# Optimization experiments

Measured on AMD Instinct MI355X. Metric: run time of the kernel, lower is better.

Reference implementation:

```python
import jax, jax.numpy as jnp
import numpy as np
from jax import lax

BS, NT, CH, K = 8, 128, 1024, 4
H = 512  # num_output_chanls // 2 per direction (bidirectional)
G = 4 * H  # gate dim, PyTorch order i,f,g,o


def setup_inputs() -> dict:
    key = jax.random.key(0)
    ks = jax.random.split(key, 9)
    s = 1.0 / np.sqrt(H)
    u = lambda k_, shape: jax.random.uniform(k_, shape, jnp.float32, -s, s)
    return {
        "inputs": jax.random.normal(ks[0], (BS, NT, CH, K), jnp.float32),
        "Wih_f": u(ks[1], (K, G, CH)),
        "Whh_f": u(ks[2], (K, G, H)),
        "bih_f": u(ks[3], (K, G)),
        "bhh_f": u(ks[4], (K, G)),
        "Wih_b": u(ks[5], (K, G, CH)),
        "Whh_b": u(ks[6], (K, G, H)),
        "bih_b": u(ks[7], (K, G)),
        "bhh_b": u(ks[8], (K, G)),
    }


def _lstm_dir(x_tbck, Wih, Whh, bih, bhh, reverse):
    # x_tbck: [nt, bs, ch, k]; weights batched over k heads.
    bs = x_tbck.shape[1]
    k, _, h = Whh.shape
    bias = bih + bhh  # [k, 4h]

    def step(carry, x_t):
        h_prev, c_prev = carry
        # detach_hidden_state=True: hidden state detached each step
        h_prev = lax.stop_gradient(h_prev)
        c_prev = lax.stop_gradient(c_prev)
        gates = (jnp.einsum('bck,kgc->bkg', x_t, Wih)
                 + jnp.einsum('bkh,kgh->bkg', h_prev, Whh)
                 + bias)  # [bs, k, 4h]
        i, f, g, o = jnp.split(gates, 4, axis=-1)
        c_new = jax.nn.sigmoid(f) * c_prev + jax.nn.sigmoid(i) * jnp.tanh(g)
        h_new = jax.nn.sigmoid(o) * jnp.tanh(c_new)
        return (h_new, c_new), h_new

    init = (jnp.zeros((bs, k, h), x_tbck.dtype), jnp.zeros((bs, k, h), x_tbck.dtype))
    _, hs = lax.scan(step, init, x_tbck, reverse=reverse)  # [nt, bs, k, h]
    return hs


def reference(inputs, Wih_f, Whh_f, bih_f, bhh_f, Wih_b, Whh_b, bih_b, bhh_b):
    # inputs: [bs, nt, ch, k] -> scan over time
    x = jnp.transpose(inputs, (1, 0, 2, 3))  # [nt, bs, ch, k]
    hs_f = _lstm_dir(x, Wih_f, Whh_f, bih_f, bhh_f, reverse=False)
    hs_b = _lstm_dir(x, Wih_b, Whh_b, bih_b, bhh_b, reverse=True)
    # [nt, bs, k, h] -> [bs, nt, h, k]; concat forward/backward on hidden dim
    hs_f = jnp.transpose(hs_f, (1, 0, 3, 2))
    hs_b = jnp.transpose(hs_b, (1, 0, 3, 2))
    return jnp.concatenate([hs_f, hs_b], axis=2)  # [bs, nt, 2h, k]
```

## Files before the change

### kernel.cpp

```cpp
#include <hip/hip_runtime.h>
#include <stdint.h>


typedef __attribute__((ext_vector_type(8))) short short8;
typedef __attribute__((ext_vector_type(4))) float floatx4;
typedef unsigned long long ull;

#define POISON 0x7FC07FC07FC07FC0ull

#define GLOAD_LDS16(g, l)                                        \
  __builtin_amdgcn_global_load_lds(                              \
      (const __attribute__((address_space(1))) void*)(g),        \
      (__attribute__((address_space(3))) void*)(l), 16, 0, 0)

__device__ __forceinline__ unsigned short f2bf(float f) {
  unsigned u = __float_as_uint(f);
  u = (u + 0x7fffu + ((u >> 16) & 1u)) >> 16;
  return (unsigned short)u;
}
__device__ __forceinline__ float sigm(float x) { return 1.0f / (1.0f + __expf(-x)); }
__device__ __forceinline__ float tanh_f(float x) {
  float ax = fabsf(x);
  float e = __expf(-2.0f * ax);
  float t = (1.0f - e) / (1.0f + e);
  return x < 0.0f ? -t : t;
}

__global__ void pack_x_k(const float* __restrict__ x, unsigned short* __restrict__ Xp) {
  int g = blockIdx.x * 256 + threadIdx.x;
  int m = g >> 10, c = g & 1023;
  int t = m >> 3, b = m & 7;
  float4 v = *(const float4*)(x + ((size_t)((b * 128 + t) * 1024 + c)) * 4);
  Xp[g]           = f2bf(v.x);
  Xp[1048576 + g] = f2bf(v.y);
  Xp[2097152 + g] = f2bf(v.z);
  Xp[3145728 + g] = f2bf(v.w);
}

__global__ void cast_bf_k(const float* __restrict__ src, unsigned short* __restrict__ dst, int n4) {
  int i = blockIdx.x * 256 + threadIdx.x;
  if (i >= n4) return;
  float4 v = ((const float4*)src)[i];
  ushort4 o;
  o.x = f2bf(v.x); o.y = f2bf(v.y); o.z = f2bf(v.z); o.w = f2bf(v.w);
  ((ushort4*)dst)[i] = o;
}

__global__ void bias_k(const float* __restrict__ bihf, const float* __restrict__ bhhf,
                       const float* __restrict__ bihb, const float* __restrict__ bhhb,
                       float* __restrict__ bias) {
  int i = blockIdx.x * 256 + threadIdx.x;
  int dk = i >> 11, g = i & 2047, kk = dk & 3;
  const float* a = (dk < 4) ? bihf : bihb;
  const float* b = (dk < 4) ? bhhf : bhhb;
  bias[i] = a[kk * 2048 + g] + b[kk * 2048 + g];
}

__global__ void fill_poison_k(ull* __restrict__ p) {
  p[(size_t)blockIdx.x * 256 + threadIdx.x] = POISON;
}

__global__ __launch_bounds__(256) void gemm_ih_k(
    const unsigned short* __restrict__ Xp, const unsigned short* __restrict__ Wb,
    const float* __restrict__ bias, float* __restrict__ ih) {
  const int mt = blockIdx.x, ntl = blockIdx.y, dk = blockIdx.z;
  const int kh = dk & 3;
  const int tid = threadIdx.x;
  const int L = tid & 63, w = tid >> 6;
  const int wm = w & 1, wn = w >> 1;
  const int quad = L >> 4, lo = L & 15;

  __shared__ unsigned short As[128 * 32];
  __shared__ unsigned short Bs[128 * 32];

  const unsigned short* Ab = Xp + (size_t)kh * 1048576 + (size_t)mt * 128 * 1024;
  const unsigned short* Bb = Wb + (size_t)dk * 2097152 + (size_t)ntl * 128 * 1024;

  floatx4 acc[4][4] = {};

  for (int kc = 0; kc < 32; ++kc) {
#pragma unroll
    for (int q = 0; q < 2; ++q) {
      int c = q * 256 + w * 64 + L;
      int ldsb = (q * 256 + w * 64) * 8;
      GLOAD_LDS16(Ab + (size_t)(c >> 2) * 1024 + kc * 32 + (c & 3) * 8, As + ldsb);
      GLOAD_LDS16(Bb + (size_t)(c >> 2) * 1024 + kc * 32 + (c & 3) * 8, Bs + ldsb);
    }
    __syncthreads();
    short8 af[4], bf[4];
#pragma unroll
    for (int mi = 0; mi < 4; ++mi)
      af[mi] = *(const short8*)(As + (wm * 64 + mi * 16 + lo) * 32 + quad * 8);
#pragma unroll
    for (int ni = 0; ni < 4; ++ni)
      bf[ni] = *(const short8*)(Bs + (wn * 64 + ni * 16 + lo) * 32 + quad * 8);
#pragma unroll
    for (int mi = 0; mi < 4; ++mi)
#pragma unroll
      for (int ni = 0; ni < 4; ++ni)
        acc[mi][ni] = __builtin_amdgcn_mfma_f32_16x16x32_bf16(af[mi], bf[ni], acc[mi][ni], 0, 0, 0);
    __syncthreads();
  }

#pragma unroll
  for (int mi = 0; mi < 4; ++mi)
#pragma unroll
    for (int ni = 0; ni < 4; ++ni) {
      int g = ntl * 128 + wn * 64 + ni * 16 + lo;
      float bv = bias[dk * 2048 + g];
#pragma unroll
      for (int r = 0; r < 4; ++r) {
        int m = mt * 128 + wm * 64 + mi * 16 + quad * 4 + r;
        ih[((size_t)dk * 1024 + m) * 2048 + g] = acc[mi][ni][r] + bv;
      }
    }
}

__global__ __launch_bounds__(256) void lstm_rec_k(
    const float* __restrict__ ih, const unsigned short* __restrict__ whh,
    float* __restrict__ out, ull* __restrict__ stateS) {
  const int tid = threadIdx.x;
  const int L = tid & 63;
  const int w = tid >> 6;
  const int grp = blockIdx.x & 7;
  const int d = grp >> 2, kh = grp & 3;
  const int wg = blockIdx.x >> 3;
  const int j0 = wg * 32;
  const int quad = L >> 4, lo = L & 15;

  __shared__ unsigned short h_lds[16 * 520];
  __shared__ float gbuf[4][8][32];

  for (int i = tid; i < 16 * 520; i += 256) h_lds[i] = 0;

  short8 bfrag[2][16];
#pragma unroll
  for (int ni = 0; ni < 2; ++ni) {
    const unsigned short* wb =
        whh + ((size_t)grp * 2048 + (size_t)(w * 512 + j0 + ni * 16 + lo)) * 512 + quad * 8;
#pragma unroll
    for (int kk = 0; kk < 16; ++kk) bfrag[ni][kk] = *(const short8*)(wb + kk * 32);
  }

  const int pb = tid >> 5, pjj = tid & 31;
  float creg = 0.0f;

  float ihv[2][4];
  {
    int t0 = d ? 127 : 0;
#pragma unroll
    for (int ni = 0; ni < 2; ++ni) {
      const float* ihp =
          ih + ((size_t)grp * 1024 + (size_t)t0 * 8) * 2048 + (w * 512 + j0 + ni * 16 + lo);
#pragma unroll
      for (int r = 0; r < 4; ++r) {
        int b = quad * 4 + r;
        ihv[ni][r] = (b < 8) ? ihp[(size_t)b * 2048] : 0.0f;
      }
    }
  }

  const int srow = tid >> 5;
  const int scol = (tid & 31) * 16;

  for (int s = 0; s < 128; ++s) {
    const int t = d ? (127 - s) : s;

    if (s) {
      const ull* src = stateS + ((size_t)grp * 128 + s) * 1024 + tid * 4;
      ull v0, v1, v2, v3;
      do {
        v0 = __hip_atomic_load(src + 0, __ATOMIC_RELAXED, __HIP_MEMORY_SCOPE_AGENT);
        v1 = __hip_atomic_load(src + 1, __ATOMIC_RELAXED, __HIP_MEMORY_SCOPE_AGENT);
        v2 = __hip_atomic_load(src + 2, __ATOMIC_RELAXED, __HIP_MEMORY_SCOPE_AGENT);
        v3 = __hip_atomic_load(src + 3, __ATOMIC_RELAXED, __HIP_MEMORY_SCOPE_AGENT);
      } while (v0 == POISON || v1 == POISON || v2 == POISON || v3 == POISON);
      unsigned short* dl = h_lds + srow * 520 + scol;
      *(ull*)(dl + 0) = v0;
      *(ull*)(dl + 4) = v1;
      *(ull*)(dl + 8) = v2;
      *(ull*)(dl + 12) = v3;
    }
    __syncthreads();

    floatx4 acc[2] = {};
    floatx4 acc2[2] = {};
    {
      const unsigned short* ar = h_lds + lo * 520 + quad * 8;
#pragma unroll
      for (int kk = 0; kk < 16; kk += 2) {
        short8 a0 = *(const short8*)(ar + kk * 32);
        short8 a1 = *(const short8*)(ar + (kk + 1) * 32);
#pragma unroll
        for (int ni = 0; ni < 2; ++ni) {
          acc[ni]  = __builtin_amdgcn_mfma_f32_16x16x32_bf16(a0, bfrag[ni][kk], acc[ni], 0, 0, 0);
          acc2[ni] = __builtin_amdgcn_mfma_f32_16x16x32_bf16(a1, bfrag[ni][kk + 1], acc2[ni], 0, 0, 0);
        }
      }
    }
#pragma unroll
    for (int ni = 0; ni < 2; ++ni)
#pragma unroll
      for (int r = 0; r < 4; ++r) {
        int b = quad * 4 + r;
        if (b < 8) gbuf[w][b][ni * 16 + lo] = acc[ni][r] + acc2[ni][r] + ihv[ni][r];
      }

    if (s < 127) {
      int tn = d ? (126 - s) : (s + 1);
#pragma unroll
      for (int ni = 0; ni < 2; ++ni) {
        const float* ihp =
            ih + ((size_t)grp * 1024 + (size_t)tn * 8) * 2048 + (w * 512 + j0 + ni * 16 + lo);
#pragma unroll
        for (int r = 0; r < 4; ++r) {
          int b = quad * 4 + r;
          ihv[ni][r] = (b < 8) ? ihp[(size_t)b * 2048] : 0.0f;
        }
      }
    }
    __syncthreads();

    {
      float ig = gbuf[0][pb][pjj], fg = gbuf[1][pb][pjj];
      float gg = gbuf[2][pb][pjj], og = gbuf[3][pb][pjj];
      float cn = sigm(fg) * creg + sigm(ig) * tanh_f(gg);
      creg = cn;
      float h = sigm(og) * tanh_f(cn);

      if (s < 127) {
        unsigned hs = f2bf(h);
        int base = L & ~3;
        unsigned v0 = __shfl(hs, base + 0);
        unsigned v1 = __shfl(hs, base + 1);
        unsigned v2 = __shfl(hs, base + 2);
        unsigned v3 = __shfl(hs, base + 3);
        if ((L & 3) == 0) {
          ull wv = (ull)v0 | ((ull)v1 << 16) | ((ull)v2 << 32) | ((ull)v3 << 48);
          ull* dst = stateS + ((size_t)grp * 128 + (s + 1)) * 1024 + pb * 128 + ((j0 + pjj) >> 2);
          __hip_atomic_store(dst, wv, __ATOMIC_RELAXED, __HIP_MEMORY_SCOPE_AGENT);
        }
      }
      out[(((size_t)pb * 128 + t) * 1024 + d * 512 + j0 + pjj) * 4 + kh] = h;
    }
  }
}

extern "C" void kernel_launch(void* const* d_in, const int* in_sizes, int n_in,
                              void* d_out, int out_size, void* d_ws, size_t ws_size,
                              hipStream_t stream) {
  (void)in_sizes; (void)n_in; (void)out_size; (void)ws_size;
  const float* x     = (const float*)d_in[0];
  const float* Wih_f = (const float*)d_in[1];
  const float* Whh_f = (const float*)d_in[2];
  const float* bih_f = (const float*)d_in[3];
  const float* bhh_f = (const float*)d_in[4];
  const float* Wih_b = (const float*)d_in[5];
  const float* Whh_b = (const float*)d_in[6];
  const float* bih_b = (const float*)d_in[7];
  const float* bhh_b = (const float*)d_in[8];
  float* out = (float*)d_out;
  char* ws = (char*)d_ws;

  float* bias          = (float*)(ws + (256u << 10));
  float* ihg           = (float*)(ws + (1ull << 20));
  unsigned short* Xp   = (unsigned short*)(ws + (65ull << 20));
  unsigned short* Wihb = (unsigned short*)(ws + (73ull << 20));
  unsigned short* Whhb = (unsigned short*)(ws + (65ull << 20));
  ull* stateS          = (ull*)(ws + (81ull << 20));

  pack_x_k<<<4096, 256, 0, stream>>>(x, Xp);
  cast_bf_k<<<8192, 256, 0, stream>>>(Wih_f, Wihb, 2097152);
  cast_bf_k<<<8192, 256, 0, stream>>>(Wih_b, Wihb + 8388608, 2097152);
  bias_k<<<64, 256, 0, stream>>>(bih_f, bhh_f, bih_b, bhh_b, bias);
  gemm_ih_k<<<dim3(8, 16, 8), 256, 0, stream>>>(Xp, Wihb, bias, ihg);
  cast_bf_k<<<4096, 256, 0, stream>>>(Whh_f, Whhb, 1048576);
  cast_bf_k<<<4096, 256, 0, stream>>>(Whh_b, Whhb + 4194304, 1048576);
  fill_poison_k<<<4096, 256, 0, stream>>>(stateS);
  lstm_rec_k<<<128, 256, 0, stream>>>(ihg, Whhb, out, stateS);
}
```

Before: 487.0 us.

## Fuse input GEMM into recurrent kernel with poison-flag streaming of gate inputs

Merges the input-projection GEMM and the recurrent LSTM kernel into one launch. Blocks 0-127 run the recurrence and the rest compute GEMM tiles, ordered by time so the forward and backward directions get their early timesteps first. The recurrent blocks poll the ih buffer, which is pre-filled with NaN poison, so the recurrence can start before the whole GEMM finishes. Bias addition is folded into the GEMM epilogue, removing the separate bias kernel. This adds a 64MB poison fill of ih and per-step polling latency, and it depends on all 128 recurrent blocks being co-resident to avoid deadlock.

```diff
diff --git a/kernel.cpp b/kernel.cpp
--- a/kernel.cpp
+++ b/kernel.cpp
@@ -7,6 +7,8 @@
 typedef unsigned long long ull;
 
 #define POISON 0x7FC07FC07FC07FC0ull
+#define POISON_F32 0x7FC00000u
+#define POISON_F32X2 0x7FC000007FC00000ull
 
 #define GLOAD_LDS16(g, l)                                        \
   __builtin_amdgcn_global_load_lds(                              \
@@ -46,90 +48,113 @@
   ((ushort4*)dst)[i] = o;
 }
 
-__global__ void bias_k(const float* __restrict__ bihf, const float* __restrict__ bhhf,
-                       const float* __restrict__ bihb, const float* __restrict__ bhhb,
-                       float* __restrict__ bias) {
-  int i = blockIdx.x * 256 + threadIdx.x;
-  int dk = i >> 11, g = i & 2047, kk = dk & 3;
-  const float* a = (dk < 4) ? bihf : bihb;
-  const float* b = (dk < 4) ? bhhf : bhhb;
-  bias[i] = a[kk * 2048 + g] + b[kk * 2048 + g];
-}
-
-__global__ void fill_poison_k(ull* __restrict__ p) {
-  p[(size_t)blockIdx.x * 256 + threadIdx.x] = POISON;
-}
-
-__global__ __launch_bounds__(256) void gemm_ih_k(
-    const unsigned short* __restrict__ Xp, const unsigned short* __restrict__ Wb,
-    const float* __restrict__ bias, float* __restrict__ ih) {
-  const int mt = blockIdx.x, ntl = blockIdx.y, dk = blockIdx.z;
-  const int kh = dk & 3;
+__global__ void fill_u64_k(ull* __restrict__ p, ull v) {
+  p[(size_t)blockIdx.x * 256 + threadIdx.x] = v;
+}
+
+__device__ __forceinline__ void poll_ih(const float* base, int quad, float ihv[2][4]) {
+  unsigned v[2][4];
+  bool ready;
+  do {
+    ready = true;
+#pragma unroll
+    for (int ni = 0; ni < 2; ++ni)
+#pragma unroll
+      for (int r = 0; r < 4; ++r) {
+        int b = quad * 4 + r;
+        if (b < 8) {
+          v[ni][r] = __hip_atomic_load((const unsigned*)base + ni * 16 + (size_t)b * 2048,
+                                       __ATOMIC_RELAXED, __HIP_MEMORY_SCOPE_AGENT);
+          if (v[ni][r] == POISON_F32) ready = false;
+        } else {
+          v[ni][r] = 0u;
+        }
+      }
+    if (!ready) __builtin_amdgcn_s_sleep(2);
+  } while (!ready);
+#pragma unroll
+  for (int ni = 0; ni < 2; ++ni)
+#pragma unroll
+    for (int r = 0; r < 4; ++r) ihv[ni][r] = __uint_as_float(v[ni][r]);
+}
+
+__global__ __launch_bounds__(256) void fused_k(
+    const unsigned short* __restrict__ Xp, const unsigned short* __restrict__ Wihb,
+    const float* __restrict__ bihf, const float* __restrict__ bhhf,
+    const float* __restrict__ bihb, const float* __restrict__ bhhb,
+    float* __restrict__ ih, const unsigned short* __restrict__ whh,
+    float* __restrict__ out, ull* __restrict__ stateS) {
+  __shared__ __align__(16) char smem[20992];
+  const int bid = blockIdx.x;
   const int tid = threadIdx.x;
-  const int L = tid & 63, w = tid >> 6;
-  const int wm = w & 1, wn = w >> 1;
+  const int L = tid & 63;
+  const int wv = tid >> 6;
   const int quad = L >> 4, lo = L & 15;
 
-  __shared__ unsigned short As[128 * 32];
-  __shared__ unsigned short Bs[128 * 32];
-
-  const unsigned short* Ab = Xp + (size_t)kh * 1048576 + (size_t)mt * 128 * 1024;
-  const unsigned short* Bb = Wb + (size_t)dk * 2097152 + (size_t)ntl * 128 * 1024;
-
-  floatx4 acc[4][4] = {};
-
-  for (int kc = 0; kc < 32; ++kc) {
-#pragma unroll
-    for (int q = 0; q < 2; ++q) {
-      int c = q * 256 + w * 64 + L;
-      int ldsb = (q * 256 + w * 64) * 8;
-      GLOAD_LDS16(Ab + (size_t)(c >> 2) * 1024 + kc * 32 + (c & 3) * 8, As + ldsb);
-      GLOAD_LDS16(Bb + (size_t)(c >> 2) * 1024 + kc * 32 + (c & 3) * 8, Bs + ldsb);
-    }
-    __syncthreads();
-    short8 af[4], bf[4];
-#pragma unroll
-    for (int mi = 0; mi < 4; ++mi)
-      af[mi] = *(const short8*)(As + (wm * 64 + mi * 16 + lo) * 32 + quad * 8);
-#pragma unroll
-    for (int ni = 0; ni < 4; ++ni)
-      bf[ni] = *(const short8*)(Bs + (wn * 64 + ni * 16 + lo) * 32 + quad * 8);
-#pragma unroll
-    for (int mi = 0; mi < 4; ++mi)
+  if (bid >= 128) {
+    const int q = bid - 128;
+    const int dk = q & 7, ntl = (q >> 3) & 15, p = q >> 7;
+    const int mt = (dk < 4) ? p : (7 - p);
+    const int kh = dk & 3;
+    const int wm = wv & 1, wn = wv >> 1;
+
+    unsigned short* As = (unsigned short*)smem;
+    unsigned short* Bs = (unsigned short*)(smem + 8192);
+
+    const unsigned short* Ab = Xp + (size_t)kh * 1048576 + (size_t)mt * 128 * 1024;
+    const unsigned short* Bb = Wihb + (size_t)dk * 2097152 + (size_t)ntl * 128 * 1024;
+
+    floatx4 acc[4][4] = {};
+
+    for (int kc = 0; kc < 32; ++kc) {
+#pragma unroll
+      for (int ph = 0; ph < 2; ++ph) {
+        int c = ph * 256 + wv * 64 + L;
+        int ldsb = (ph * 256 + wv * 64) * 8;
+        GLOAD_LDS16(Ab + (size_t)(c >> 2) * 1024 + kc * 32 + (c & 3) * 8, As + ldsb);
+        GLOAD_LDS16(Bb + (size_t)(c >> 2) * 1024 + kc * 32 + (c & 3) * 8, Bs + ldsb);
+      }
+      __syncthreads();
+      short8 af[4], bf[4];
+#pragma unroll
+      for (int mi = 0; mi < 4; ++mi)
+        af[mi] = *(const short8*)(As + (wm * 64 + mi * 16 + lo) * 32 + quad * 8);
 #pragma unroll
       for (int ni = 0; ni < 4; ++ni)
-        acc[mi][ni] = __builtin_amdgcn_mfma_f32_16x16x32_bf16(af[mi], bf[ni], acc[mi][ni], 0, 0, 0);
-    __syncthreads();
-  }
-
-#pragma unroll
-  for (int mi = 0; mi < 4; ++mi)
+        bf[ni] = *(const short8*)(Bs + (wn * 64 + ni * 16 + lo) * 32 + quad * 8);
+#pragma unroll
+      for (int mi = 0; mi < 4; ++mi)
+#pragma unroll
+        for (int ni = 0; ni < 4; ++ni)
+          acc[mi][ni] = __builtin_amdgcn_mfma_f32_16x16x32_bf16(af[mi], bf[ni], acc[mi][ni], 0, 0, 0);
+      __syncthreads();
+    }
+
+    const float* bihp = (dk < 4) ? bihf : bihb;
+    const float* bhhp = (dk < 4) ? bhhf : bhhb;
 #pragma unroll
     for (int ni = 0; ni < 4; ++ni) {
       int g = ntl * 128 + wn * 64 + ni * 16 + lo;
-      float bv = bias[dk * 2048 + g];
-#pragma unroll
-      for (int r = 0; r < 4; ++r) {
-        int m = mt * 128 + wm * 64 + mi * 16 + quad * 4 + r;
-        ih[((size_t)dk * 1024 + m) * 2048 + g] = acc[mi][ni][r] + bv;
-      }
-    }
-}
-
-__global__ __launch_bounds__(256) void lstm_rec_k(
-    const float* __restrict__ ih, const unsigned short* __restrict__ whh,
-    float* __restrict__ out, ull* __restrict__ stateS) {
-  const int tid = threadIdx.x;
-  const int L = tid & 63;
-  const int w = tid >> 6;
-  const int grp = blockIdx.x & 7;
+      float bv = bihp[kh * 2048 + g] + bhhp[kh * 2048 + g];
+#pragma unroll
+      for (int mi = 0; mi < 4; ++mi)
+#pragma unroll
+        for (int r = 0; r < 4; ++r) {
+          int m = mt * 128 + wm * 64 + mi * 16 + quad * 4 + r;
+          __hip_atomic_store(&ih[((size_t)dk * 1024 + m) * 2048 + g], acc[mi][ni][r] + bv,
+                             __ATOMIC_RELAXED, __HIP_MEMORY_SCOPE_AGENT);
+        }
+    }
+    return;
+  }
+
+  const int grp = bid & 7;
   const int d = grp >> 2, kh = grp & 3;
-  const int wg = blockIdx.x >> 3;
+  const int wg = bid >> 3;
   const int j0 = wg * 32;
-  const int quad = L >> 4, lo = L & 15;
-
-  __shared__ unsigned short h_lds[16 * 520];
-  __shared__ float gbuf[4][8][32];
+
+  unsigned short* h_lds = (unsigned short*)smem;
+  float* gbuf = (float*)(smem + 16640);
 
   for (int i = tid; i < 16 * 520; i += 256) h_lds[i] = 0;
 
@@ -137,7 +162,7 @@
 #pragma unroll
   for (int ni = 0; ni < 2; ++ni) {
     const unsigned short* wb =
-        whh + ((size_t)grp * 2048 + (size_t)(w * 512 + j0 + ni * 16 + lo)) * 512 + quad * 8;
+        whh + ((size_t)grp * 2048 + (size_t)(wv * 512 + j0 + ni * 16 + lo)) * 512 + quad * 8;
 #pragma unroll
     for (int kk = 0; kk < 16; ++kk) bfrag[ni][kk] = *(const short8*)(wb + kk * 32);
   }
@@ -148,16 +173,9 @@
   float ihv[2][4];
   {
     int t0 = d ? 127 : 0;
-#pragma unroll
-    for (int ni = 0; ni < 2; ++ni) {
-      const float* ihp =
-          ih + ((size_t)grp * 1024 + (size_t)t0 * 8) * 2048 + (w * 512 + j0 + ni * 16 + lo);
-#pragma unroll
-      for (int r = 0; r < 4; ++r) {
-        int b = quad * 4 + r;
-        ihv[ni][r] = (b < 8) ? ihp[(size_t)b * 2048] : 0.0f;
-      }
-    }
+    const float* base =
+        ih + ((size_t)grp * 1024 + (size_t)t0 * 8) * 2048 + (wv * 512 + j0 + lo);
+    poll_ih(base, quad, ihv);
   }
 
   const int srow = tid >> 5;
@@ -203,27 +221,13 @@
 #pragma unroll
       for (int r = 0; r < 4; ++r) {
         int b = quad * 4 + r;
-        if (b < 8) gbuf[w][b][ni * 16 + lo] = acc[ni][r] + acc2[ni][r] + ihv[ni][r];
-      }
-
-    if (s < 127) {
-      int tn = d ? (126 - s) : (s + 1);
-#pragma unroll
-      for (int ni = 0; ni < 2; ++ni) {
-        const float* ihp =
-            ih + ((size_t)grp * 1024 + (size_t)tn * 8) * 2048 + (w * 512 + j0 + ni * 16 + lo);
-#pragma unroll
-        for (int r = 0; r < 4; ++r) {
-          int b = quad * 4 + r;
-          ihv[ni][r] = (b < 8) ? ihp[(size_t)b * 2048] : 0.0f;
-        }
-      }
-    }
+        if (b < 8) gbuf[((wv * 8) + b) * 32 + ni * 16 + lo] = acc[ni][r] + acc2[ni][r] + ihv[ni][r];
+      }
     __syncthreads();
 
     {
-      float ig = gbuf[0][pb][pjj], fg = gbuf[1][pb][pjj];
-      float gg = gbuf[2][pb][pjj], og = gbuf[3][pb][pjj];
+      float ig = gbuf[(0 * 8 + pb) * 32 + pjj], fg = gbuf[(1 * 8 + pb) * 32 + pjj];
+      float gg = gbuf[(2 * 8 + pb) * 32 + pjj], og = gbuf[(3 * 8 + pb) * 32 + pjj];
       float cn = sigm(fg) * creg + sigm(ig) * tanh_f(gg);
       creg = cn;
       float h = sigm(og) * tanh_f(cn);
@@ -236,12 +240,19 @@
         unsigned v2 = __shfl(hs, base + 2);
         unsigned v3 = __shfl(hs, base + 3);
         if ((L & 3) == 0) {
-          ull wv = (ull)v0 | ((ull)v1 << 16) | ((ull)v2 << 32) | ((ull)v3 << 48);
+          ull wvv = (ull)v0 | ((ull)v1 << 16) | ((ull)v2 << 32) | ((ull)v3 << 48);
           ull* dst = stateS + ((size_t)grp * 128 + (s + 1)) * 1024 + pb * 128 + ((j0 + pjj) >> 2);
-          __hip_atomic_store(dst, wv, __ATOMIC_RELAXED, __HIP_MEMORY_SCOPE_AGENT);
+          __hip_atomic_store(dst, wvv, __ATOMIC_RELAXED, __HIP_MEMORY_SCOPE_AGENT);
         }
       }
       out[(((size_t)pb * 128 + t) * 1024 + d * 512 + j0 + pjj) * 4 + kh] = h;
+    }
+
+    if (s < 127) {
+      int tn = d ? (126 - s) : (s + 1);
+      const float* base =
+          ih + ((size_t)grp * 1024 + (size_t)tn * 8) * 2048 + (wv * 512 + j0 + lo);
+      poll_ih(base, quad, ihv);
     }
   }
 }
@@ -262,20 +273,19 @@
   float* out = (float*)d_out;
   char* ws = (char*)d_ws;
 
-  float* bias          = (float*)(ws + (256u << 10));
-  float* ihg           = (float*)(ws + (1ull << 20));
-  unsigned short* Xp   = (unsigned short*)(ws + (65ull << 20));
-  unsigned short* Wihb = (unsigned short*)(ws + (73ull << 20));
-  unsigned short* Whhb = (unsigned short*)(ws + (65ull << 20));
-  ull* stateS          = (ull*)(ws + (81ull << 20));
+  ull* stateS          = (ull*)ws;
+  float* ihg           = (float*)(ws + (8ull << 20));
+  unsigned short* Xp   = (unsigned short*)(ws + (72ull << 20));
+  unsigned short* Wihb = (unsigned short*)(ws + (80ull << 20));
+  unsigned short* Whhb = (unsigned short*)(ws + (112ull << 20));
 
   pack_x_k<<<4096, 256, 0, stream>>>(x, Xp);
   cast_bf_k<<<8192, 256, 0, stream>>>(Wih_f, Wihb, 2097152);
   cast_bf_k<<<8192, 256, 0, stream>>>(Wih_b, Wihb + 8388608, 2097152);
-  bias_k<<<64, 256, 0, stream>>>(bih_f, bhh_f, bih_b, bhh_b, bias);
-  gemm_ih_k<<<dim3(8, 16, 8), 256, 0, stream>>>(Xp, Wihb, bias, ihg);
   cast_bf_k<<<4096, 256, 0, stream>>>(Whh_f, Whhb, 1048576);
   cast_bf_k<<<4096, 256, 0, stream>>>(Whh_b, Whhb + 4194304, 1048576);
-  fill_poison_k<<<4096, 256, 0, stream>>>(stateS);
-  lstm_rec_k<<<128, 256, 0, stream>>>(ihg, Whhb, out, stateS);
-}
+  fill_u64_k<<<4096, 256, 0, stream>>>(stateS, POISON);
+  fill_u64_k<<<32768, 256, 0, stream>>>((ull*)ihg, POISON_F32X2);
+  fused_k<<<1152, 256, 0, stream>>>(Xp, Wihb, bih_f, bhh_f, bih_b, bhh_b,
+                                    ihg, Whhb, out, stateS);
+}
```

Result: slower. 585.1 us (+20.1%).
